# Optimization experiments

Measured on AMD Instinct MI355X. Metric: run time of the kernel, lower is better.

Reference implementation:

```python
import jax, jax.numpy as jnp
import numpy as np

DELTA_AGG = 0.5
MAX_T = 16  # instance ids in [0, MAX_T); 0 = background


def setup_inputs() -> dict:
    key = jax.random.key(0)
    k1, k2 = jax.random.split(key)
    preds = jax.random.normal(k1, (32, 6, 256, 256), dtype=jnp.float32)
    targets = jax.random.randint(k2, (32, 2, 256, 256), 0, MAX_T, dtype=jnp.int32)
    return {"preds": preds, "targets": targets}


def _per_sample_loss(sim_b, text_b, kernel_b):
    # sim_b: [4, P] similarity vectors; text_b/kernel_b: [P] int instance ids
    ones = jnp.ones_like(text_b, dtype=sim_b.dtype)
    # kernel segment stats -> per-instance mean similarity vector G_Ki
    k_cnt = jax.ops.segment_sum(ones, kernel_b, num_segments=MAX_T)          # [MAX_T]
    k_sum = jax.ops.segment_sum(sim_b.T, kernel_b, num_segments=MAX_T)       # [MAX_T, 4]
    G = k_sum / jnp.maximum(k_cnt, 1.0)[:, None]                             # [MAX_T, 4]
    # text segment counts
    t_cnt = jax.ops.segment_sum(ones, text_b, num_segments=MAX_T)            # [MAX_T]
    # per-pixel distance to the kernel mean of its own text instance
    Gp = G[text_b]                                                           # [P, 4]
    d = jnp.linalg.norm(sim_b.T - Gp, axis=1) - DELTA_AGG                    # [P]
    loss_pix = jnp.log(jnp.square(jnp.maximum(d, 0.0)) + 1.0)                # [P]
    inst_sum = jax.ops.segment_sum(loss_pix, text_b, num_segments=MAX_T)     # [MAX_T]
    ids = jnp.arange(MAX_T)
    valid = (ids >= 1) & (k_cnt > 0) & (t_cnt > 0)                           # skip bg & empty instances
    inst_mean = jnp.where(valid, inst_sum / jnp.maximum(t_cnt, 1.0), 0.0)
    n_valid = jnp.sum(valid.astype(sim_b.dtype))
    return jnp.where(n_valid > 0, jnp.sum(inst_mean) / jnp.maximum(n_valid, 1.0), 0.0)


def reference(preds, targets):
    N = preds.shape[0]
    sim = preds[:, 2:, :, :].reshape(N, 4, -1)       # [N, 4, P]
    text = targets[:, 0].reshape(N, -1)              # [N, P]
    kernel = targets[:, 1].reshape(N, -1)            # [N, P]
    return jax.vmap(_per_sample_loss)(sim, text, kernel)  # [N]
```

## Files before the change

kernel.cpp:

```cpp
#include <hip/hip_runtime.h>
#include <hip/hip_bf16.h>


#define P_PIX 65536
#define NS 32
#define NB1 32
#define NB2 32
#define SP_F 96
#define WS_STATS_OFF 0
#define WS_LP_OFF (NS * NB1 * SP_F)
#define WS_SC_OFF (WS_LP_OFF + NS * NB2)

typedef float v2f __attribute__((ext_vector_type(2)));

template <int CTRL, int RM>
__device__ __forceinline__ float dpp_mov_f(float v) {
    return __int_as_float(
        __builtin_amdgcn_update_dpp(0, __float_as_int(v), CTRL, RM, 0xf, true));
}
template <int CTRL, int RM>
__device__ __forceinline__ int dpp_mov_i(int v) {
    return __builtin_amdgcn_update_dpp(0, v, CTRL, RM, 0xf, true);
}
__device__ __forceinline__ float wave_sum_f(float v) {
    v += dpp_mov_f<0x111, 0xf>(v);
    v += dpp_mov_f<0x112, 0xf>(v);
    v += dpp_mov_f<0x114, 0xf>(v);
    v += dpp_mov_f<0x118, 0xf>(v);
    v += dpp_mov_f<0x142, 0xa>(v);
    v += dpp_mov_f<0x143, 0xc>(v);
    return v;
}
__device__ __forceinline__ unsigned int wave_sum_u(unsigned int v) {
    v += (unsigned int)dpp_mov_i<0x111, 0xf>((int)v);
    v += (unsigned int)dpp_mov_i<0x112, 0xf>((int)v);
    v += (unsigned int)dpp_mov_i<0x114, 0xf>((int)v);
    v += (unsigned int)dpp_mov_i<0x118, 0xf>((int)v);
    v += (unsigned int)dpp_mov_i<0x142, 0xa>((int)v);
    v += (unsigned int)dpp_mov_i<0x143, 0xc>((int)v);
    return v;
}


#define ROWF 34

__global__ __launch_bounds__(128) void agg_stats_kernel(
        const float* __restrict__ preds,
        const int* __restrict__ targets,
        float* __restrict__ ws) {
    const int s = blockIdx.y;
    const int b = blockIdx.x;
    const int tid = threadIdx.x;
    const int lane = tid & 63;
    const int w = tid >> 6;

    __shared__ __align__(16) float acc[2][128][ROWF];
    {
        float4* a4 = (float4*)acc;
        #pragma unroll
        for (int i = 0; i < 17; ++i)
            a4[i * 128 + tid] = make_float4(0.f, 0.f, 0.f, 0.f);
    }
    __syncthreads();

    unsigned long long kp[2] = {0ull, 0ull}, tp[2] = {0ull, 0ull};

    const float* sim  = preds + (size_t)s * 6 * P_PIX + 2 * (size_t)P_PIX;
    const int*   text = targets + (size_t)s * 2 * P_PIX;
    const int*   kern = text + P_PIX;

    float* row01 = &acc[0][tid][0];
    float* row23 = &acc[1][tid][0];

    #pragma unroll
    for (int it = 0; it < 4; ++it) {
        const int p4 = b * 512 + it * 128 + tid;
        const int4   tb4 = ((const int4*)text)[p4];
        const int4   kb4 = ((const int4*)kern)[p4];
        const float4 v0 = ((const float4*)(sim))[p4];
        const float4 v1 = ((const float4*)(sim + P_PIX))[p4];
        const float4 v2 = ((const float4*)(sim + 2 * P_PIX))[p4];
        const float4 v3 = ((const float4*)(sim + 3 * P_PIX))[p4];
        const int tbv[4] = {tb4.x, tb4.y, tb4.z, tb4.w};
        const int kbv[4] = {kb4.x, kb4.y, kb4.z, kb4.w};
        const v2f a01[4] = {{v0.x, v1.x}, {v0.y, v1.y}, {v0.z, v1.z}, {v0.w, v1.w}};
        const v2f a23[4] = {{v2.x, v3.x}, {v2.y, v3.y}, {v2.z, v3.z}, {v2.w, v3.w}};
        const int h = it >> 1;
        #pragma unroll
        for (int j = 0; j < 4; ++j) {
            const int kb = kbv[j], tb = tbv[j];
            kp[h] += 1ull << (4 * kb);
            tp[h] += 1ull << (4 * tb);
            v2f* p01 = (v2f*)&row01[kb * 2];
            v2f* p23 = (v2f*)&row23[kb * 2];
            *p01 = *p01 + a01[j];
            *p23 = *p23 + a23[j];
        }
    }

    const unsigned long long M4 = 0x0F0F0F0F0F0F0F0Full;
    const unsigned long long M8 = 0x00FF00FF00FF00FFull;
    unsigned int kc[8], tc[8];
    {
        unsigned long long e = (kp[0] & M4) + (kp[1] & M4);
        unsigned long long o = ((kp[0] >> 4) & M4) + ((kp[1] >> 4) & M4);
        unsigned long long e0 = e & M8, e1 = (e >> 8) & M8;
        unsigned long long o0 = o & M8, o1 = (o >> 8) & M8;
        kc[0] = (unsigned int)e0; kc[1] = (unsigned int)(e0 >> 32);
        kc[2] = (unsigned int)e1; kc[3] = (unsigned int)(e1 >> 32);
        kc[4] = (unsigned int)o0; kc[5] = (unsigned int)(o0 >> 32);
        kc[6] = (unsigned int)o1; kc[7] = (unsigned int)(o1 >> 32);
    }
    {
        unsigned long long e = (tp[0] & M4) + (tp[1] & M4);
        unsigned long long o = ((tp[0] >> 4) & M4) + ((tp[1] >> 4) & M4);
        unsigned long long e0 = e & M8, e1 = (e >> 8) & M8;
        unsigned long long o0 = o & M8, o1 = (o >> 8) & M8;
        tc[0] = (unsigned int)e0; tc[1] = (unsigned int)(e0 >> 32);
        tc[2] = (unsigned int)e1; tc[3] = (unsigned int)(e1 >> 32);
        tc[4] = (unsigned int)o0; tc[5] = (unsigned int)(o0 >> 32);
        tc[6] = (unsigned int)o1; tc[7] = (unsigned int)(o1 >> 32);
    }
    #pragma unroll
    for (int k = 0; k < 8; ++k) { kc[k] = wave_sum_u(kc[k]); tc[k] = wave_sum_u(tc[k]); }

    __shared__ unsigned int wk[2][8], wt[2][8];
    __shared__ float colred[64][2];
    if (lane == 63) {
        #pragma unroll
        for (int k = 0; k < 8; ++k) { wk[w][k] = kc[k]; wt[w][k] = tc[k]; }
    }
    __syncthreads();

    {
        const int col = tid & 63;
        const int q = tid >> 6;
        const int bin = col >> 2, ch = col & 3;
        const int region = ch >> 1, sub = ch & 1;
        float sum = 0.0f;
        #pragma unroll 16
        for (int r = 0; r < 64; ++r)
            sum += acc[region][q * 64 + r][bin * 2 + sub];
        colred[col][q] = sum;
    }
    __syncthreads();

    float* part = ws + WS_STATS_OFF + (size_t)(s * NB1 + b) * SP_F;
    if (tid < 64) {
        const int bin = tid >> 2, ch = tid & 3;
        if (bin >= 1)
            part[15 + (bin - 1) * 4 + ch] = colred[tid][0] + colred[tid][1];
    } else if (tid >= 64 && tid < 94) {
        const int k = tid - 64;
        const int bin = (k < 15) ? (k + 1) : (k - 14);
        const unsigned int (*src)[8] = (k < 15) ? wk : wt;
        const int u = (bin & 1) * 2 + ((bin >> 1) & 1);
        const int f = bin >> 2;
        const int idx = u * 2 + (f >> 1);
        const int sh = (f & 1) * 16;
        const unsigned int sum = src[0][idx] + src[1][idx];
        part[(k < 15) ? k : (75 + k - 15)] = (float)((sum >> sh) & 0xFFFFu);
    }
}


__global__ __launch_bounds__(256) void agg_loss_kernel(
        const float* __restrict__ preds,
        const int* __restrict__ targets,
        float* __restrict__ ws) {
    const int s = blockIdx.y;
    const int b = blockIdx.x;
    const int tid = threadIdx.x;
    const int lane = tid & 63;
    const int w = tid >> 6;

    __shared__ float tmp[90];
    __shared__ __align__(16) float4 G4[16];
    __shared__ float w16[16];
    __shared__ float ip[4];

    if (tid < 90) {
        const float* base = ws + WS_STATS_OFF + (size_t)s * NB1 * SP_F + tid;
        float v = 0.0f;
        #pragma unroll 8
        for (int pb = 0; pb < NB1; ++pb) v += base[pb * SP_F];
        tmp[tid] = v;
    }
    __syncthreads();
    if (tid < 60) ((float*)G4)[4 + tid] = tmp[15 + tid] / fmaxf(tmp[tid >> 2], 1.0f);
    if (tid >= 64 && tid < 68) ((float*)G4)[tid - 64] = 0.0f;
    if (tid < 16) {
        if (tid == 15) {
            w16[0] = 0.0f;
        } else {
            const float kcv = tmp[tid];
            const float tcv = tmp[75 + tid];
            w16[tid + 1] = (kcv > 0.0f && tcv > 0.0f) ? 1.0f / tcv : 0.0f;
        }
    }
    if (w == 0) {
        const bool vld = (tid < 15) && (tmp[tid] > 0.0f) && (tmp[75 + tid] > 0.0f);
        const unsigned long long m = __ballot(vld);
        if (b == 0 && tid == 0) {
            const float nv = (float)__popcll(m);
            ws[WS_SC_OFF + s] = (nv > 0.0f) ? 1.0f / nv : 0.0f;
        }
    }
    __syncthreads();

    const float* sim  = preds + (size_t)s * 6 * P_PIX + 2 * (size_t)P_PIX;
    const int*   text = targets + (size_t)s * 2 * P_PIX;

    float racc = 0.0f;
    #pragma unroll
    for (int it = 0; it < 2; ++it) {
        const int p4 = b * 512 + it * 256 + tid;
        const int4   tb4 = ((const int4*)text)[p4];
        const float4 v0 = ((const float4*)(sim))[p4];
        const float4 v1 = ((const float4*)(sim + P_PIX))[p4];
        const float4 v2 = ((const float4*)(sim + 2 * P_PIX))[p4];
        const float4 v3 = ((const float4*)(sim + 3 * P_PIX))[p4];
        const int tbv[4] = {tb4.x, tb4.y, tb4.z, tb4.w};
        const float a[4][4] = {{v0.x, v1.x, v2.x, v3.x}, {v0.y, v1.y, v2.y, v3.y},
                               {v0.z, v1.z, v2.z, v3.z}, {v0.w, v1.w, v2.w, v3.w}};
        #pragma unroll
        for (int j = 0; j < 4; ++j) {
            const int tb = tbv[j];
            const float4 g = G4[tb];
            const float wv = w16[tb];
            const float d0 = a[j][0] - g.x;
            const float d1 = a[j][1] - g.y;
            const float d2 = a[j][2] - g.z;
            const float d3 = a[j][3] - g.w;
            const float dd = sqrtf(d0 * d0 + d1 * d1 + d2 * d2 + d3 * d3) - 0.5f;
            const float r = fmaxf(dd, 0.0f);
            const float lp = __logf(fmaf(r, r, 1.0f));
            racc = fmaf(lp, wv, racc);
        }
    }

    racc = wave_sum_f(racc);
    if (lane == 63) ip[w] = racc;
    __syncthreads();
    if (tid == 0)
        ws[WS_LP_OFF + (size_t)s * NB2 + b] = (ip[0] + ip[1]) + (ip[2] + ip[3]);
}


__global__ __launch_bounds__(64) void agg_final_kernel(
        const float* __restrict__ ws, float* __restrict__ out) {
    const int s = blockIdx.x;
    const int tid = threadIdx.x;
    float v = (tid < NB2) ? ws[WS_LP_OFF + (size_t)s * NB2 + tid] : 0.0f;
    #pragma unroll
    for (int off = 32; off >= 1; off >>= 1) v += __shfl_down(v, off);
    if (tid == 0) out[s] = v * ws[WS_SC_OFF + s];
}

extern "C" void kernel_launch(void* const* d_in, const int* in_sizes, int n_in,
                              void* d_out, int out_size, void* d_ws, size_t ws_size,
                              hipStream_t stream) {
    const float* preds = (const float*)d_in[0];
    const int* targets = (const int*)d_in[1];
    float* out = (float*)d_out;
    float* ws = (float*)d_ws;

    agg_stats_kernel<<<dim3(NB1, NS), 128, 0, stream>>>(preds, targets, ws);
    agg_loss_kernel<<<dim3(NB2, NS), 256, 0, stream>>>(preds, targets, ws);
    agg_final_kernel<<<NS, 64, 0, stream>>>(ws, out);
}
```

Baseline: 24.87 us.

## Drop final reduction kernel via atomics and double loss-kernel grid

The separate final reduction launch is removed. Each loss block now scales its partial sum by the per-sample 1/n_valid and atomically adds it into the output, which the stats kernel zeroes first. The loss kernel grid doubles so each block handles one iteration instead of two, and the stats reduction is split across two thread groups. This saves one kernel launch and adds parallelism, at the cost of float atomics (non-deterministic summation order) and redundant per-block stats reduction.

Result: slower. 38.80 us (+56.0%).

```diff
diff --git a/kernel.cpp b/kernel.cpp
--- a/kernel.cpp
+++ b/kernel.cpp
@@ -5,11 +5,9 @@
 #define P_PIX 65536
 #define NS 32
 #define NB1 32
-#define NB2 32
+#define NB2 64
 #define SP_F 96
 #define WS_STATS_OFF 0
-#define WS_LP_OFF (NS * NB1 * SP_F)
-#define WS_SC_OFF (WS_LP_OFF + NS * NB2)
 
 typedef float v2f __attribute__((ext_vector_type(2)));
 
@@ -47,12 +45,15 @@
 __global__ __launch_bounds__(128) void agg_stats_kernel(
         const float* __restrict__ preds,
         const int* __restrict__ targets,
-        float* __restrict__ ws) {
+        float* __restrict__ ws,
+        float* __restrict__ out) {
     const int s = blockIdx.y;
     const int b = blockIdx.x;
     const int tid = threadIdx.x;
     const int lane = tid & 63;
     const int w = tid >> 6;
+
+    if (b == 0 && tid == 0) out[s] = 0.0f;
 
     __shared__ __align__(16) float acc[2][128][ROWF];
     {
@@ -167,25 +168,32 @@
 __global__ __launch_bounds__(256) void agg_loss_kernel(
         const float* __restrict__ preds,
         const int* __restrict__ targets,
-        float* __restrict__ ws) {
+        const float* __restrict__ ws,
+        float* __restrict__ out) {
     const int s = blockIdx.y;
     const int b = blockIdx.x;
     const int tid = threadIdx.x;
     const int lane = tid & 63;
     const int w = tid >> 6;
 
+    __shared__ float tmp2[2][90];
     __shared__ float tmp[90];
     __shared__ __align__(16) float4 G4[16];
     __shared__ float w16[16];
     __shared__ float ip[4];
-
-    if (tid < 90) {
-        const float* base = ws + WS_STATS_OFF + (size_t)s * NB1 * SP_F + tid;
-        float v = 0.0f;
-        #pragma unroll 8
-        for (int pb = 0; pb < NB1; ++pb) v += base[pb * SP_F];
-        tmp[tid] = v;
-    }
+    __shared__ float sscale;
+
+    if (tid < 180) {
+        const int c = (tid >= 90) ? 1 : 0;
+        const int v = tid - c * 90;
+        const float* base = ws + WS_STATS_OFF + (size_t)s * NB1 * SP_F + v;
+        float a = 0.0f;
+        #pragma unroll
+        for (int pb = c * 16; pb < c * 16 + 16; ++pb) a += base[pb * SP_F];
+        tmp2[c][v] = a;
+    }
+    __syncthreads();
+    if (tid < 90) tmp[tid] = tmp2[0][tid] + tmp2[1][tid];
     __syncthreads();
     if (tid < 60) ((float*)G4)[4 + tid] = tmp[15 + tid] / fmaxf(tmp[tid >> 2], 1.0f);
     if (tid >= 64 && tid < 68) ((float*)G4)[tid - 64] = 0.0f;
@@ -198,13 +206,12 @@
             w16[tid + 1] = (kcv > 0.0f && tcv > 0.0f) ? 1.0f / tcv : 0.0f;
         }
     }
-    if (w == 0) {
-        const bool vld = (tid < 15) && (tmp[tid] > 0.0f) && (tmp[75 + tid] > 0.0f);
-        const unsigned long long m = __ballot(vld);
-        if (b == 0 && tid == 0) {
-            const float nv = (float)__popcll(m);
-            ws[WS_SC_OFF + s] = (nv > 0.0f) ? 1.0f / nv : 0.0f;
-        }
+    if (tid == 0) {
+        float nv = 0.0f;
+        #pragma unroll
+        for (int t = 0; t < 15; ++t)
+            nv += (tmp[t] > 0.0f && tmp[75 + t] > 0.0f) ? 1.0f : 0.0f;
+        sscale = (nv > 0.0f) ? 1.0f / nv : 0.0f;
     }
     __syncthreads();
 
@@ -212,9 +219,8 @@
     const int*   text = targets + (size_t)s * 2 * P_PIX;
 
     float racc = 0.0f;
-    #pragma unroll
-    for (int it = 0; it < 2; ++it) {
-        const int p4 = b * 512 + it * 256 + tid;
+    {
+        const int p4 = b * 256 + tid;
         const int4   tb4 = ((const int4*)text)[p4];
         const float4 v0 = ((const float4*)(sim))[p4];
         const float4 v1 = ((const float4*)(sim + P_PIX))[p4];
@@ -242,19 +248,10 @@
     racc = wave_sum_f(racc);
     if (lane == 63) ip[w] = racc;
     __syncthreads();
-    if (tid == 0)
-        ws[WS_LP_OFF + (size_t)s * NB2 + b] = (ip[0] + ip[1]) + (ip[2] + ip[3]);
-}
-
-
-__global__ __launch_bounds__(64) void agg_final_kernel(
-        const float* __restrict__ ws, float* __restrict__ out) {
-    const int s = blockIdx.x;
-    const int tid = threadIdx.x;
-    float v = (tid < NB2) ? ws[WS_LP_OFF + (size_t)s * NB2 + tid] : 0.0f;
-    #pragma unroll
-    for (int off = 32; off >= 1; off >>= 1) v += __shfl_down(v, off);
-    if (tid == 0) out[s] = v * ws[WS_SC_OFF + s];
+    if (tid == 0) {
+        const float blocksum = (ip[0] + ip[1]) + (ip[2] + ip[3]);
+        atomicAdd(&out[s], blocksum * sscale);
+    }
 }
 
 extern "C" void kernel_launch(void* const* d_in, const int* in_sizes, int n_in,
@@ -265,7 +262,6 @@
     float* out = (float*)d_out;
     float* ws = (float*)d_ws;
 
-    agg_stats_kernel<<<dim3(NB1, NS), 128, 0, stream>>>(preds, targets, ws);
-    agg_loss_kernel<<<dim3(NB2, NS), 256, 0, stream>>>(preds, targets, ws);
-    agg_final_kernel<<<NS, 64, 0, stream>>>(ws, out);
-}
+    agg_stats_kernel<<<dim3(NB1, NS), 128, 0, stream>>>(preds, targets, ws, out);
+    agg_loss_kernel<<<dim3(NB2, NS), 256, 0, stream>>>(preds, targets, ws, out);
+}
```
